# Performance work log

Measured on AMD Instinct MI355X. Metric: run time of the kernel, lower is better.

Reference implementation:

```python
import jax, jax.numpy as jnp
import numpy as np


def _edt_background(gt):
    """Exact Euclidean distance transform of (1 - gt): distance from each pixel
    to the nearest foreground (gt==1) pixel. gt: [H, W] int. Returns [H, W] f32.
    Separable formulation: g(i,j) = 1D distance along row i to nearest fg;
    D(i,j)^2 = min_{i'} ( (i-i')^2 + g(i',j)^2 ), which is the exact 2D EDT.
    """
    H, W = gt.shape
    BIG = jnp.float32(H + W)  # upper bound on any true distance
    fg = gt > 0
    col = jnp.arange(W, dtype=jnp.float32)
    # nearest fg index to the left (running max of fg column index)
    left = jax.lax.cummax(jnp.where(fg, col, -BIG), axis=1)
    d_left = col[None, :] - left
    # nearest fg index to the right: running max of (-col) from the right = -min(col)
    right = jax.lax.cummax(jnp.where(fg, -col, -BIG)[:, ::-1], axis=1)[:, ::-1]
    d_right = (-right) - col[None, :]
    g = jnp.clip(jnp.minimum(d_left, d_right), 0.0, BIG)  # [H, W] 1D row distances
    g2 = g * g
    row = jnp.arange(H, dtype=jnp.float32)
    di2 = (row[:, None] - row[None, :]) ** 2              # [H, H]
    d2 = jnp.min(di2[:, :, None] + g2[None, :, :], axis=1)  # [H, W]
    return jnp.sqrt(d2)


def setup_inputs() -> dict:
    key = jax.random.key(0)
    k1, k2 = jax.random.split(key)
    B, H, W = 16, 384, 384
    logits = jax.random.normal(k1, (B, 1, H, W), dtype=jnp.float32)
    targets = jax.random.randint(k2, (B, 1, H, W), 0, 2).astype(jnp.int32)
    return {"logits": logits, "targets": targets}


def reference(logits, targets):
    probs = jax.nn.sigmoid(logits)            # [B,1,H,W]
    gt = targets[:, 0]                        # [B,H,W] int
    # sequential map over batch keeps the [H,H,W] EDT intermediate per-sample
    dist = jax.lax.map(_edt_background, gt)   # [B,H,W] f32
    tgt_f = gt.astype(jnp.float32)
    per_sample = jnp.mean(jnp.abs(probs[:, 0] - tgt_f) * dist, axis=(1, 2))
    return jnp.mean(per_sample)
```

## Files before the change

### kernel.cpp

```cpp
#include <hip/hip_runtime.h>
#include <math.h>


#define BB 16
#define HH 384
#define WW 384
#define WPR 12
#define WPRP 13
#define SW 8
#define NBLK (WW / SW)
#define THREADS 256
#define BIGD 768

__global__ __launch_bounds__(THREADS) void pack_kernel(
    const int* __restrict__ gt, unsigned* __restrict__ mask,
    float* __restrict__ out) {
  const int idx = blockIdx.x * THREADS + threadIdx.x;
  const bool fg = gt[idx] != 0;
  const unsigned long long m = __ballot(fg);
  const int lane = threadIdx.x & 63;
  if (lane == 0) mask[idx >> 5] = (unsigned)m;
  else if (lane == 32) mask[idx >> 5] = (unsigned)(m >> 32);
  if (idx == 0) out[0] = 0.0f;
}

__global__ __launch_bounds__(THREADS) void boundary_loss_kernel(
    const float* __restrict__ logits, const unsigned* __restrict__ mask,
    float* __restrict__ out) {
  const int blk = blockIdx.x;
  const int b = blk / NBLK;
  const int j0 = (blk % NBLK) * SW;
  const float* __restrict__ lg = logits + b * HH * WW;

  __shared__ unsigned m_s[HH * WPRP];
  __shared__ unsigned short g_s[HH * SW];

  const uint4* __restrict__ gm4 = (const uint4*)(mask + b * HH * WPR);
  for (int s = threadIdx.x; s < HH * WPR / 4; s += THREADS) {
    const uint4 v = gm4[s];
    const int row = s / 3;
    const int w0 = (s - row * 3) * 4;
    unsigned* dst = m_s + row * WPRP + w0;
    dst[0] = v.x; dst[1] = v.y; dst[2] = v.z; dst[3] = v.w;
  }
  __syncthreads();

  for (int s = threadIdx.x; s < HH * 2; s += THREADS) {
    const int i = s >> 1;
    const int jj = (s & 1) * 4;
    const int j = j0 + jj;
    const unsigned* __restrict__ mr = m_s + i * WPRP;
    const int w = j >> 5;
    const int bpos = j & 31;
    const unsigned cur = mr[w];

    int jL = -0x40000;
    if ((cur & (0xFFFFFFFFu >> (31 - bpos))) == 0u) {
      for (int ww = w - 1; ww >= 0; --ww) {
        const unsigned x = mr[ww];
        if (x) { jL = ww * 32 + 31 - __clz(x); break; }
      }
    }
    int jR = 0x40000;
    if ((cur & (0xFFFFFFFFu << (bpos + 3))) == 0u) {
      for (int ww = w + 1; ww < WPR; ++ww) {
        const unsigned x = mr[ww];
        if (x) { jR = ww * 32 + __ffs(x) - 1; break; }
      }
    }
    unsigned short g4[4];
#pragma unroll
    for (int c = 0; c < 4; ++c) {
      const int bc = bpos + c;
      const int jc = j + c;
      const unsigned lm = cur & (0xFFFFFFFFu >> (31 - bc));
      const unsigned rm = cur & (0xFFFFFFFFu << bc);
      const int dl = lm ? (bc - (31 - __clz(lm))) : (jc - jL);
      const int dr = rm ? ((__ffs(rm) - 1) - bc) : (jR - jc);
      g4[c] = (unsigned short)min(min(dl, dr), BIGD);
    }
    ushort4 gv; gv.x = g4[0]; gv.y = g4[1]; gv.z = g4[2]; gv.w = g4[3];
    *(ushort4*)(g_s + i * SW + jj) = gv;
  }
  __syncthreads();

  float acc = 0.0f;
  for (int s = threadIdx.x; s < HH * 2; s += THREADS) {
    const int i = s >> 1;
    const int jj = (s & 1) * 4;
    const ushort4 gv = *(const ushort4*)(g_s + i * SW + jj);
    const float4 x4 = *(const float4*)(lg + i * WW + j0 + jj);
    const int gg[4] = {gv.x, gv.y, gv.z, gv.w};
    const float xs[4] = {x4.x, x4.y, x4.z, x4.w};
#pragma unroll
    for (int c = 0; c < 4; ++c) {
      int best = gg[c] * gg[c];
      for (int r = 1; r * r < best; ++r) {
        const int im = i - r, ip = i + r;
        if (im >= 0) { const int v = g_s[im * SW + jj + c]; best = min(best, r * r + v * v); }
        if (ip < HH) { const int v = g_s[ip * SW + jj + c]; best = min(best, r * r + v * v); }
      }
      const float dist = sqrtf((float)best);
      const float p = 1.0f / (1.0f + __expf(-xs[c]));
      acc += p * dist;
    }
  }

  __shared__ float red[THREADS / 64];
  for (int off = 32; off > 0; off >>= 1) acc += __shfl_down(acc, off, 64);
  const int lane = threadIdx.x & 63;
  const int wid = threadIdx.x >> 6;
  if (lane == 0) red[wid] = acc;
  __syncthreads();
  if (threadIdx.x == 0) {
    float ssum = 0.0f;
    for (int w = 0; w < THREADS / 64; ++w) ssum += red[w];
    atomicAdd(out, ssum * (1.0f / (float)(BB * HH * WW)));
  }
}

extern "C" void kernel_launch(void* const* d_in, const int* in_sizes, int n_in,
                              void* d_out, int out_size, void* d_ws, size_t ws_size,
                              hipStream_t stream) {
  const float* logits = (const float*)d_in[0];
  const int* targets = (const int*)d_in[1];
  float* out = (float*)d_out;
  unsigned* mask = (unsigned*)d_ws;

  pack_kernel<<<(BB * HH * WW) / THREADS, THREADS, 0, stream>>>(targets, mask, out);
  boundary_loss_kernel<<<BB * NBLK, THREADS, 0, stream>>>(logits, mask, out);
}
```

Measured before the change: 82.28 us.

## Vectorize mask packing, widen column strips, use fast sqrt and rcp

The mask pack kernel now loads eight targets per thread with int4 loads and assembles 32-bit words via shared-memory bytes instead of wave ballots. The main kernel processes 16-column strips with 512 threads, halving the number of blocks and the redundant per-block mask reloads. Sigmoid and sqrt use hardware rcp/sqrt intrinsics. The wider strips reduce grid parallelism and may change occupancy; the intrinsics trade slight precision.

```diff
diff --git a/kernel.cpp b/kernel.cpp
--- a/kernel.cpp
+++ b/kernel.cpp
@@ -7,21 +7,29 @@
 #define WW 384
 #define WPR 12
 #define WPRP 13
-#define SW 8
+#define SW 16
 #define NBLK (WW / SW)
-#define THREADS 256
+#define THREADS 512
+#define PTHREADS 256
 #define BIGD 768
 
-__global__ __launch_bounds__(THREADS) void pack_kernel(
+__global__ __launch_bounds__(PTHREADS) void pack_kernel(
     const int* __restrict__ gt, unsigned* __restrict__ mask,
     float* __restrict__ out) {
-  const int idx = blockIdx.x * THREADS + threadIdx.x;
-  const bool fg = gt[idx] != 0;
-  const unsigned long long m = __ballot(fg);
-  const int lane = threadIdx.x & 63;
-  if (lane == 0) mask[idx >> 5] = (unsigned)m;
-  else if (lane == 32) mask[idx >> 5] = (unsigned)(m >> 32);
-  if (idx == 0) out[0] = 0.0f;
+  __shared__ unsigned char s_byte[PTHREADS];
+  const int base = blockIdx.x * PTHREADS * 8;
+  const int4* __restrict__ g4 = (const int4*)(gt + base);
+  const int4 a = g4[threadIdx.x * 2];
+  const int4 b = g4[threadIdx.x * 2 + 1];
+  unsigned byte = (a.x != 0) | ((a.y != 0) << 1) | ((a.z != 0) << 2) |
+                  ((a.w != 0) << 3) | ((b.x != 0) << 4) | ((b.y != 0) << 5) |
+                  ((b.z != 0) << 6) | ((b.w != 0) << 7);
+  s_byte[threadIdx.x] = (unsigned char)byte;
+  __syncthreads();
+  if (threadIdx.x < PTHREADS / 4) {
+    mask[(base >> 5) + threadIdx.x] = *(const unsigned*)(s_byte + threadIdx.x * 4);
+  }
+  if (blockIdx.x == 0 && threadIdx.x == 0) out[0] = 0.0f;
 }
 
 __global__ __launch_bounds__(THREADS) void boundary_loss_kernel(
@@ -45,9 +53,9 @@
   }
   __syncthreads();
 
-  for (int s = threadIdx.x; s < HH * 2; s += THREADS) {
-    const int i = s >> 1;
-    const int jj = (s & 1) * 4;
+  for (int s = threadIdx.x; s < HH * (SW / 4); s += THREADS) {
+    const int i = s >> 2;
+    const int jj = (s & 3) * 4;
     const int j = j0 + jj;
     const unsigned* __restrict__ mr = m_s + i * WPRP;
     const int w = j >> 5;
@@ -85,9 +93,9 @@
   __syncthreads();
 
   float acc = 0.0f;
-  for (int s = threadIdx.x; s < HH * 2; s += THREADS) {
-    const int i = s >> 1;
-    const int jj = (s & 1) * 4;
+  for (int s = threadIdx.x; s < HH * (SW / 4); s += THREADS) {
+    const int i = s >> 2;
+    const int jj = (s & 3) * 4;
     const ushort4 gv = *(const ushort4*)(g_s + i * SW + jj);
     const float4 x4 = *(const float4*)(lg + i * WW + j0 + jj);
     const int gg[4] = {gv.x, gv.y, gv.z, gv.w};
@@ -100,8 +108,8 @@
         if (im >= 0) { const int v = g_s[im * SW + jj + c]; best = min(best, r * r + v * v); }
         if (ip < HH) { const int v = g_s[ip * SW + jj + c]; best = min(best, r * r + v * v); }
       }
-      const float dist = sqrtf((float)best);
-      const float p = 1.0f / (1.0f + __expf(-xs[c]));
+      const float dist = __builtin_amdgcn_sqrtf((float)best);
+      const float p = __builtin_amdgcn_rcpf(1.0f + __expf(-xs[c]));
       acc += p * dist;
     }
   }
@@ -127,6 +135,6 @@
   float* out = (float*)d_out;
   unsigned* mask = (unsigned*)d_ws;
 
-  pack_kernel<<<(BB * HH * WW) / THREADS, THREADS, 0, stream>>>(targets, mask, out);
+  pack_kernel<<<(BB * HH * WW) / (PTHREADS * 8), PTHREADS, 0, stream>>>(targets, mask, out);
   boundary_loss_kernel<<<BB * NBLK, THREADS, 0, stream>>>(logits, mask, out);
 }
```

Result: faster. 75.50 us (-8.2%).
